# Kernel tuning notes

Hardware: AMD Instinct MI355X
Metric: run time of the kernel (lower is better)

## Reference

```python
import jax, jax.numpy as jnp
import numpy as np

WINDOW_SIZE = 11
SIGMA = 1.5
C1 = 0.01 ** 2
C2 = 0.03 ** 2


def _gaussian_window(window_size: int, channel: int) -> jnp.ndarray:
    # 1D gaussian, normalized
    g = jnp.arange(window_size, dtype=jnp.float32) - window_size // 2
    g = jnp.exp(-(g ** 2) / (2.0 * SIGMA ** 2))
    g = g / g.sum()
    w2d = jnp.outer(g, g)  # [K, K]
    # depthwise conv kernel: [C, 1, K, K] in OIHW with feature_group_count=C
    return jnp.broadcast_to(w2d[None, None], (channel, 1, window_size, window_size))


def _depthwise_conv(x: jnp.ndarray, window: jnp.ndarray, channel: int) -> jnp.ndarray:
    pad = WINDOW_SIZE // 2
    return jax.lax.conv_general_dilated(
        x, window,
        window_strides=(1, 1),
        padding=((pad, pad), (pad, pad)),
        dimension_numbers=('NCHW', 'OIHW', 'NCHW'),
        feature_group_count=channel,
    )


def setup_inputs() -> dict:
    key = jax.random.key(0)
    k1, k2 = jax.random.split(key)
    shape = (16, 3, 512, 512)
    img1 = jax.random.uniform(k1, shape, dtype=jnp.float32)
    img2 = jax.random.uniform(k2, shape, dtype=jnp.float32)
    return {"img1": img1, "img2": img2}


def reference(img1, img2):
    channel = img1.shape[1]
    window = _gaussian_window(WINDOW_SIZE, channel).astype(img1.dtype)

    mu1 = _depthwise_conv(img1, window, channel)
    mu2 = _depthwise_conv(img2, window, channel)

    mu1_sq = mu1 * mu1
    mu2_sq = mu2 * mu2
    mu1_mu2 = mu1 * mu2

    sigma1_sq = _depthwise_conv(img1 * img1, window, channel) - mu1_sq
    sigma2_sq = _depthwise_conv(img2 * img2, window, channel) - mu2_sq
    sigma12 = _depthwise_conv(img1 * img2, window, channel) - mu1_mu2

    ssim_map = ((2.0 * mu1_mu2 + C1) * (2.0 * sigma12 + C2)) / (
        (mu1_sq + mu2_sq + C1) * (sigma1_sq + sigma2_sq + C2))

    return 1.0 - ssim_map.mean()
```

## Files before the change

### kernel.cpp

```cpp
#include <hip/hip_runtime.h>

#define IMG_W 512
#define IMG_H 512
#define PLANE_PX (IMG_W * IMG_H)
#define N_ELEMS (48 * PLANE_PX)
#define NTHREADS 256
#define TILEW 48
#define NCT 11
#define NBANDS 8
#define NBLK (48 * NBANDS * NCT)

#define C1x2 2.0e-4f
#define C2x2 1.8e-3f

typedef _Float16 h2 __attribute__((ext_vector_type(2)));
typedef _Float16 h8 __attribute__((ext_vector_type(8)));
typedef float f32x4 __attribute__((ext_vector_type(4)));
typedef __fp16 fp16v2 __attribute__((ext_vector_type(2)));

__device__ __forceinline__ unsigned int h2bits(h2 v) {
    union { h2 h; unsigned int u; } c; c.h = v; return c.u;
}
__device__ __forceinline__ h2 pkrtz(float x, float y) {
    union { fp16v2 f; h2 h; } c;
    c.f = __builtin_amdgcn_cvt_pkrtz(x, y);
    return c.h;
}

__global__ void __launch_bounds__(NTHREADS, 5) ssim_main(
    const float* __restrict__ img1, const float* __restrict__ img2,
    float* __restrict__ partials)
{
    __shared__ __align__(16) unsigned short P[4 * 64 * 64];

    const int tid = threadIdx.x;
    const int lane = tid & 63;
    const int wv = tid >> 6;
    const int nr = lane & 15;
    const int khi = lane >> 4;

    const int xcd = blockIdx.x & 7;
    const int idx = blockIdx.x >> 3;
    const int pl = xcd * 6 + idx / 88;
    const int t = idx % 88;
    const int band = t / 11;
    const int ct = t - band * 11;
    const int tx0 = ct * TILEW;
    const int ty0 = band * 64;
    const float* pa = img1 + (size_t)pl * PLANE_PX;
    const float* pb = img2 + (size_t)pl * PLANE_PX;

    int sidx = min(lane, 10 - lane);
    unsigned gvb = 0u;
    gvb = (sidx == 0) ? 0x1436u : gvb;
    gvb = (sidx == 1) ? 0x1FC8u : gvb;
    gvb = (sidx == 2) ? 0x289Cu : gvb;
    gvb = (sidx == 3) ? 0x2F00u : gvb;
    gvb = (sidx == 4) ? 0x32D1u : gvb;
    gvb = (sidx == 5) ? 0x3442u : gvb;
    union { h8 h; unsigned u[4]; } af;
#pragma unroll
    for (int w = 0; w < 4; ++w) {
        int t0 = khi * 8 + 2 * w - nr;
        unsigned lo = (unsigned)__shfl((int)gvb, t0 & 63, 64);
        unsigned hi = (unsigned)__shfl((int)gvb, (t0 + 1) & 63, 64);
        af.u[w] = (lo & 0xFFFFu) | (hi << 16);
    }

    const f32x4 z = {0.f, 0.f, 0.f, 0.f};

    const int ry0 = ty0 + wv * 16 - 5;
    const int ryb = ry0 + khi * 8;
    const bool fastY = (ry0 >= 0) && (ry0 + 31 < IMG_H);
    const bool edge = (ct == 0) || (ct == NCT - 1);

#pragma unroll
    for (int tc = 0; tc < 4; ++tc) {
        const int gx = tx0 - 5 + tc * 16 + nr;
        const int cgx = min(max(gx, 0), IMG_W - 1);
        float s[8], d[8];
        if (fastY) {
            const float* qa = pa + (size_t)ryb * IMG_W + cgx;
            const float* qb = pb + (size_t)ryb * IMG_W + cgx;
#pragma unroll
            for (int j = 0; j < 8; ++j) {
                float a = qa[j * IMG_W], b = qb[j * IMG_W];
                s[j] = a + b; d[j] = a - b;
            }
        } else {
#pragma unroll
            for (int j = 0; j < 8; ++j) {
                int ry = ryb + j;
                int ryc = min(max(ry, 0), IMG_H - 1);
                float rm = ((unsigned)ry < (unsigned)IMG_H) ? 1.f : 0.f;
                float a = pa[(size_t)ryc * IMG_W + cgx] * rm;
                float b = pb[(size_t)ryc * IMG_W + cgx] * rm;
                s[j] = a + b; d[j] = a - b;
            }
        }
        union { h8 h; h2 p[4]; } FS, FD, FSS, FDD;
#pragma unroll
        for (int w = 0; w < 4; ++w) {
            FS.p[w] = pkrtz(s[2 * w], s[2 * w + 1]);
            FD.p[w] = pkrtz(d[2 * w], d[2 * w + 1]);
        }
        if (edge) {
            const _Float16 ml = ((unsigned)gx < (unsigned)IMG_W) ? (_Float16)1.f
                                                                 : (_Float16)0.f;
            const h2 mlv = {ml, ml};
#pragma unroll
            for (int w = 0; w < 4; ++w) { FS.p[w] *= mlv; FD.p[w] *= mlv; }
        }
#pragma unroll
        for (int w = 0; w < 4; ++w) {
            FSS.p[w] = FS.p[w] * FS.p[w];
            FDD.p[w] = FD.p[w] * FD.p[w];
        }
        f32x4 oS  = __builtin_amdgcn_mfma_f32_16x16x32_f16(FS.h,  af.h, z, 0, 0, 0);
        f32x4 oD  = __builtin_amdgcn_mfma_f32_16x16x32_f16(FD.h,  af.h, z, 0, 0, 0);
        f32x4 oSS = __builtin_amdgcn_mfma_f32_16x16x32_f16(FSS.h, af.h, z, 0, 0, 0);
        f32x4 oDD = __builtin_amdgcn_mfma_f32_16x16x32_f16(FDD.h, af.h, z, 0, 0, 0);

        const int prow = wv * 16 + nr;
        const int swc = (tc * 16 + khi * 4) ^ ((nr & 7) << 3);
        unsigned short* q = &P[prow * 64 + swc];
        *(uint2*)(q)         = make_uint2(h2bits(pkrtz(oS[0],  oS[1])),
                                          h2bits(pkrtz(oS[2],  oS[3])));
        *(uint2*)(q + 4096)  = make_uint2(h2bits(pkrtz(oD[0],  oD[1])),
                                          h2bits(pkrtz(oD[2],  oD[3])));
        *(uint2*)(q + 8192)  = make_uint2(h2bits(pkrtz(oSS[0], oSS[1])),
                                          h2bits(pkrtz(oSS[2], oSS[3])));
        *(uint2*)(q + 12288) = make_uint2(h2bits(pkrtz(oDD[0], oDD[1])),
                                          h2bits(pkrtz(oDD[2], oDD[3])));
    }
    __syncthreads();

    const int row = wv * 16 + nr;
    float local = 0.f;
#pragma unroll
    for (int mg = 0; mg < 3; ++mg) {
        if (tx0 + mg * 16 < IMG_W) {
            const int gi = ((mg * 2 + khi) ^ (nr & 7)) * 8;
            const unsigned short* base = &P[row * 64 + gi];
            h8 fS  = *(const h8*)(base);
            h8 fD  = *(const h8*)(base + 4096);
            h8 fSS = *(const h8*)(base + 8192);
            h8 fDD = *(const h8*)(base + 12288);
            f32x4 aS  = __builtin_amdgcn_mfma_f32_16x16x32_f16(af.h, fS,  z, 0, 0, 0);
            f32x4 aD  = __builtin_amdgcn_mfma_f32_16x16x32_f16(af.h, fD,  z, 0, 0, 0);
            f32x4 aSS = __builtin_amdgcn_mfma_f32_16x16x32_f16(af.h, fSS, z, 0, 0, 0);
            f32x4 aDD = __builtin_amdgcn_mfma_f32_16x16x32_f16(af.h, fDD, z, 0, 0, 0);

#pragma unroll
            for (int i = 0; i < 4; ++i) {
                float cs = aS[i], cd = aD[i], css = aSS[i], cdd = aDD[i];
                float Pq = cs * cs, Qq = cd * cd;
                float U = Pq - Qq;
                float V = Pq + Qq;
                float num = (U + C1x2) * ((css - cdd) - U + C2x2);
                float den = (V + C1x2) * ((css + cdd) - V + C2x2);
                local += num * __builtin_amdgcn_rcpf(den);
            }
        }
    }

#pragma unroll
    for (int off = 32; off > 0; off >>= 1) local += __shfl_down(local, off, 64);
    __syncthreads();
    float* wp = (float*)P;
    if (lane == 0) wp[wv] = local;
    __syncthreads();
    if (tid == 0)
        partials[blockIdx.x] = wp[0] + wp[1] + wp[2] + wp[3];
}

__global__ void ssim_final(const float* __restrict__ partials,
                           float* __restrict__ out)
{
    __shared__ float wp[4];
    const int tid = threadIdx.x;
    const float4* p4 = (const float4*)partials;
    float s = 0.f;
    for (int i = tid; i < NBLK / 4; i += NTHREADS) {
        float4 v = p4[i];
        s += (v.x + v.y) + (v.z + v.w);
    }
#pragma unroll
    for (int off = 32; off > 0; off >>= 1) s += __shfl_down(s, off, 64);
    if ((tid & 63) == 0) wp[tid >> 6] = s;
    __syncthreads();
    if (tid == 0)
        out[0] = 1.0f - (wp[0] + wp[1] + wp[2] + wp[3]) * (1.0f / (float)N_ELEMS);
}

extern "C" void kernel_launch(void* const* d_in, const int* in_sizes, int n_in,
                              void* d_out, int out_size, void* d_ws, size_t ws_size,
                              hipStream_t stream) {
    const float* img1 = (const float*)d_in[0];
    const float* img2 = (const float*)d_in[1];
    float* out = (float*)d_out;
    float* partials = (float*)d_ws;

    ssim_main<<<NBLK, NTHREADS, 0, stream>>>(img1, img2, partials);
    ssim_final<<<1, NTHREADS, 0, stream>>>(partials, out);
}
```

Baseline: 134.7 us.

## Keep separable blur in registers per wave, removing LDS staging and block sync

Each wave now owns a 16x64 output strip and runs the vertical MFMA on two column groups. It feeds the fp16 results straight back as the B operand of a horizontal MFMA, using a shifted weight fragment, so no shared-memory staging is needed. This removes the LDS round-trip, the __syncthreads barriers and the block-level reduction, and each wave writes its own partial sum. In exchange, halo loads are redundant across the 16-column groups, more global loads are issued per output, and the per-wave loop is not unrolled.

```diff
diff --git a/kernel.cpp b/kernel.cpp
--- a/kernel.cpp
+++ b/kernel.cpp
@@ -5,10 +5,8 @@
 #define PLANE_PX (IMG_W * IMG_H)
 #define N_ELEMS (48 * PLANE_PX)
 #define NTHREADS 256
-#define TILEW 48
-#define NCT 11
-#define NBANDS 8
-#define NBLK (48 * NBANDS * NCT)
+#define NBLK 3072
+#define NWAVES (NBLK * 4)
 
 #define C1x2 2.0e-4f
 #define C2x2 1.8e-3f
@@ -27,26 +25,24 @@
     return c.h;
 }
 
-__global__ void __launch_bounds__(NTHREADS, 5) ssim_main(
+union FrU { h8 h; unsigned u[4]; h2 p[4]; };
+
+__global__ void __launch_bounds__(NTHREADS, 4) ssim_main(
     const float* __restrict__ img1, const float* __restrict__ img2,
     float* __restrict__ partials)
 {
-    __shared__ __align__(16) unsigned short P[4 * 64 * 64];
-
     const int tid = threadIdx.x;
     const int lane = tid & 63;
     const int wv = tid >> 6;
     const int nr = lane & 15;
     const int khi = lane >> 4;
 
-    const int xcd = blockIdx.x & 7;
-    const int idx = blockIdx.x >> 3;
-    const int pl = xcd * 6 + idx / 88;
-    const int t = idx % 88;
-    const int band = t / 11;
-    const int ct = t - band * 11;
-    const int tx0 = ct * TILEW;
-    const int ty0 = band * 64;
+    const int bswz = (blockIdx.x & 7) * (NBLK / 8) + (blockIdx.x >> 3);
+    const int wid = bswz * 4 + wv;
+    const int pl = wid >> 8;
+    const int r = wid & 255;
+    const int oy0 = (r >> 3) * 16;
+    const int sx0 = (r & 7) * 64;
     const float* pa = img1 + (size_t)pl * PLANE_PX;
     const float* pb = img2 + (size_t)pl * PLANE_PX;
 
@@ -58,120 +54,134 @@
     gvb = (sidx == 3) ? 0x2F00u : gvb;
     gvb = (sidx == 4) ? 0x32D1u : gvb;
     gvb = (sidx == 5) ? 0x3442u : gvb;
-    union { h8 h; unsigned u[4]; } af;
+    FrU afv, afh;
 #pragma unroll
     for (int w = 0; w < 4; ++w) {
         int t0 = khi * 8 + 2 * w - nr;
         unsigned lo = (unsigned)__shfl((int)gvb, t0 & 63, 64);
         unsigned hi = (unsigned)__shfl((int)gvb, (t0 + 1) & 63, 64);
-        af.u[w] = (lo & 0xFFFFu) | (hi << 16);
+        afv.u[w] = (lo & 0xFFFFu) | (hi << 16);
+        unsigned lo2 = (unsigned)__shfl((int)gvb, (t0 - 3) & 63, 64);
+        unsigned hi2 = (unsigned)__shfl((int)gvb, (t0 - 2) & 63, 64);
+        afh.u[w] = (lo2 & 0xFFFFu) | (hi2 << 16);
     }
 
+    const int ry0 = oy0 - 5;
+    const int ryb = ry0 + khi * 8;
+    const bool fastY = (ry0 >= 0) && (ry0 + 25 < IMG_H);
+    const int colo = ((nr >> 2) << 3) + (nr & 3);
+
     const f32x4 z = {0.f, 0.f, 0.f, 0.f};
-
-    const int ry0 = ty0 + wv * 16 - 5;
-    const int ryb = ry0 + khi * 8;
-    const bool fastY = (ry0 >= 0) && (ry0 + 31 < IMG_H);
-    const bool edge = (ct == 0) || (ct == NCT - 1);
-
-#pragma unroll
-    for (int tc = 0; tc < 4; ++tc) {
-        const int gx = tx0 - 5 + tc * 16 + nr;
-        const int cgx = min(max(gx, 0), IMG_W - 1);
-        float s[8], d[8];
+    float local = 0.f;
+
+#pragma unroll 1
+    for (int mg = 0; mg < 4; ++mg) {
+        const int ox0 = sx0 + mg * 16;
+        const int wx = ox0 - 8;
+        const int c0 = wx + colo;
+        const int c1 = c0 + 4;
+        const bool edgeC = (wx < 0) || (wx + 32 > IMG_W);
+        const int cc0 = min(max(c0, 0), IMG_W - 1);
+        const int cc1 = min(max(c1, 0), IMG_W - 1);
+
+        float a0[8], b0[8], a1[8], b1[8];
+#pragma unroll
+        for (int j = 0; j < 8; ++j) { a0[j] = 0.f; b0[j] = 0.f; a1[j] = 0.f; b1[j] = 0.f; }
+#define LOADJ_FAST(j) { \
+            a0[j] = qa[(j) * IMG_W + cc0]; b0[j] = qb[(j) * IMG_W + cc0]; \
+            a1[j] = qa[(j) * IMG_W + cc1]; b1[j] = qb[(j) * IMG_W + cc1]; }
+#define LOADJ_EDGE(j) { \
+            int ry = ryb + (j); \
+            int ryc = min(max(ry, 0), IMG_H - 1); \
+            float rm = ((unsigned)ry < (unsigned)IMG_H) ? 1.f : 0.f; \
+            a0[j] = pa[(size_t)ryc * IMG_W + cc0] * rm; \
+            b0[j] = pb[(size_t)ryc * IMG_W + cc0] * rm; \
+            a1[j] = pa[(size_t)ryc * IMG_W + cc1] * rm; \
+            b1[j] = pb[(size_t)ryc * IMG_W + cc1] * rm; }
         if (fastY) {
-            const float* qa = pa + (size_t)ryb * IMG_W + cgx;
-            const float* qb = pb + (size_t)ryb * IMG_W + cgx;
-#pragma unroll
-            for (int j = 0; j < 8; ++j) {
-                float a = qa[j * IMG_W], b = qb[j * IMG_W];
-                s[j] = a + b; d[j] = a - b;
+            const float* qa = pa + (size_t)ryb * IMG_W;
+            const float* qb = pb + (size_t)ryb * IMG_W;
+            LOADJ_FAST(0) LOADJ_FAST(1)
+            if (khi != 3) {
+#pragma unroll
+                for (int j = 2; j < 8; ++j) LOADJ_FAST(j)
             }
         } else {
-#pragma unroll
-            for (int j = 0; j < 8; ++j) {
-                int ry = ryb + j;
-                int ryc = min(max(ry, 0), IMG_H - 1);
-                float rm = ((unsigned)ry < (unsigned)IMG_H) ? 1.f : 0.f;
-                float a = pa[(size_t)ryc * IMG_W + cgx] * rm;
-                float b = pb[(size_t)ryc * IMG_W + cgx] * rm;
-                s[j] = a + b; d[j] = a - b;
+            LOADJ_EDGE(0) LOADJ_EDGE(1)
+            if (khi != 3) {
+#pragma unroll
+                for (int j = 2; j < 8; ++j) LOADJ_EDGE(j)
             }
         }
-        union { h8 h; h2 p[4]; } FS, FD, FSS, FDD;
+#undef LOADJ_FAST
+#undef LOADJ_EDGE
+
+        FrU FS0, FD0, FS1, FD1;
 #pragma unroll
         for (int w = 0; w < 4; ++w) {
-            FS.p[w] = pkrtz(s[2 * w], s[2 * w + 1]);
-            FD.p[w] = pkrtz(d[2 * w], d[2 * w + 1]);
-        }
-        if (edge) {
-            const _Float16 ml = ((unsigned)gx < (unsigned)IMG_W) ? (_Float16)1.f
-                                                                 : (_Float16)0.f;
-            const h2 mlv = {ml, ml};
-#pragma unroll
-            for (int w = 0; w < 4; ++w) { FS.p[w] *= mlv; FD.p[w] *= mlv; }
-        }
+            FS0.p[w] = pkrtz(a0[2 * w] + b0[2 * w], a0[2 * w + 1] + b0[2 * w + 1]);
+            FD0.p[w] = pkrtz(a0[2 * w] - b0[2 * w], a0[2 * w + 1] - b0[2 * w + 1]);
+            FS1.p[w] = pkrtz(a1[2 * w] + b1[2 * w], a1[2 * w + 1] + b1[2 * w + 1]);
+            FD1.p[w] = pkrtz(a1[2 * w] - b1[2 * w], a1[2 * w + 1] - b1[2 * w + 1]);
+        }
+        if (edgeC) {
+            const _Float16 m0 = ((unsigned)c0 < (unsigned)IMG_W) ? (_Float16)1.f : (_Float16)0.f;
+            const _Float16 m1 = ((unsigned)c1 < (unsigned)IMG_W) ? (_Float16)1.f : (_Float16)0.f;
+            const h2 m0v = {m0, m0}, m1v = {m1, m1};
+#pragma unroll
+            for (int w = 0; w < 4; ++w) {
+                FS0.p[w] *= m0v; FD0.p[w] *= m0v;
+                FS1.p[w] *= m1v; FD1.p[w] *= m1v;
+            }
+        }
+        FrU FSS0, FDD0, FSS1, FDD1;
 #pragma unroll
         for (int w = 0; w < 4; ++w) {
-            FSS.p[w] = FS.p[w] * FS.p[w];
-            FDD.p[w] = FD.p[w] * FD.p[w];
-        }
-        f32x4 oS  = __builtin_amdgcn_mfma_f32_16x16x32_f16(FS.h,  af.h, z, 0, 0, 0);
-        f32x4 oD  = __builtin_amdgcn_mfma_f32_16x16x32_f16(FD.h,  af.h, z, 0, 0, 0);
-        f32x4 oSS = __builtin_amdgcn_mfma_f32_16x16x32_f16(FSS.h, af.h, z, 0, 0, 0);
-        f32x4 oDD = __builtin_amdgcn_mfma_f32_16x16x32_f16(FDD.h, af.h, z, 0, 0, 0);
-
-        const int prow = wv * 16 + nr;
-        const int swc = (tc * 16 + khi * 4) ^ ((nr & 7) << 3);
-        unsigned short* q = &P[prow * 64 + swc];
-        *(uint2*)(q)         = make_uint2(h2bits(pkrtz(oS[0],  oS[1])),
-                                          h2bits(pkrtz(oS[2],  oS[3])));
-        *(uint2*)(q + 4096)  = make_uint2(h2bits(pkrtz(oD[0],  oD[1])),
-                                          h2bits(pkrtz(oD[2],  oD[3])));
-        *(uint2*)(q + 8192)  = make_uint2(h2bits(pkrtz(oSS[0], oSS[1])),
-                                          h2bits(pkrtz(oSS[2], oSS[3])));
-        *(uint2*)(q + 12288) = make_uint2(h2bits(pkrtz(oDD[0], oDD[1])),
-                                          h2bits(pkrtz(oDD[2], oDD[3])));
+            FSS0.p[w] = FS0.p[w] * FS0.p[w];
+            FDD0.p[w] = FD0.p[w] * FD0.p[w];
+            FSS1.p[w] = FS1.p[w] * FS1.p[w];
+            FDD1.p[w] = FD1.p[w] * FD1.p[w];
+        }
+
+        f32x4 oS0  = __builtin_amdgcn_mfma_f32_16x16x32_f16(FS0.h,  afv.h, z, 0, 0, 0);
+        f32x4 oD0  = __builtin_amdgcn_mfma_f32_16x16x32_f16(FD0.h,  afv.h, z, 0, 0, 0);
+        f32x4 oSS0 = __builtin_amdgcn_mfma_f32_16x16x32_f16(FSS0.h, afv.h, z, 0, 0, 0);
+        f32x4 oDD0 = __builtin_amdgcn_mfma_f32_16x16x32_f16(FDD0.h, afv.h, z, 0, 0, 0);
+        f32x4 oS1  = __builtin_amdgcn_mfma_f32_16x16x32_f16(FS1.h,  afv.h, z, 0, 0, 0);
+        f32x4 oD1  = __builtin_amdgcn_mfma_f32_16x16x32_f16(FD1.h,  afv.h, z, 0, 0, 0);
+        f32x4 oSS1 = __builtin_amdgcn_mfma_f32_16x16x32_f16(FSS1.h, afv.h, z, 0, 0, 0);
+        f32x4 oDD1 = __builtin_amdgcn_mfma_f32_16x16x32_f16(FDD1.h, afv.h, z, 0, 0, 0);
+
+        FrU bS, bD, bSS, bDD;
+        bS.u[0]  = h2bits(pkrtz(oS0[0],  oS0[1]));  bS.u[1]  = h2bits(pkrtz(oS0[2],  oS0[3]));
+        bS.u[2]  = h2bits(pkrtz(oS1[0],  oS1[1]));  bS.u[3]  = h2bits(pkrtz(oS1[2],  oS1[3]));
+        bD.u[0]  = h2bits(pkrtz(oD0[0],  oD0[1]));  bD.u[1]  = h2bits(pkrtz(oD0[2],  oD0[3]));
+        bD.u[2]  = h2bits(pkrtz(oD1[0],  oD1[1]));  bD.u[3]  = h2bits(pkrtz(oD1[2],  oD1[3]));
+        bSS.u[0] = h2bits(pkrtz(oSS0[0], oSS0[1])); bSS.u[1] = h2bits(pkrtz(oSS0[2], oSS0[3]));
+        bSS.u[2] = h2bits(pkrtz(oSS1[0], oSS1[1])); bSS.u[3] = h2bits(pkrtz(oSS1[2], oSS1[3]));
+        bDD.u[0] = h2bits(pkrtz(oDD0[0], oDD0[1])); bDD.u[1] = h2bits(pkrtz(oDD0[2], oDD0[3]));
+        bDD.u[2] = h2bits(pkrtz(oDD1[0], oDD1[1])); bDD.u[3] = h2bits(pkrtz(oDD1[2], oDD1[3]));
+
+        f32x4 aS  = __builtin_amdgcn_mfma_f32_16x16x32_f16(afh.h, bS.h,  z, 0, 0, 0);
+        f32x4 aD  = __builtin_amdgcn_mfma_f32_16x16x32_f16(afh.h, bD.h,  z, 0, 0, 0);
+        f32x4 aSS = __builtin_amdgcn_mfma_f32_16x16x32_f16(afh.h, bSS.h, z, 0, 0, 0);
+        f32x4 aDD = __builtin_amdgcn_mfma_f32_16x16x32_f16(afh.h, bDD.h, z, 0, 0, 0);
+
+#pragma unroll
+        for (int i = 0; i < 4; ++i) {
+            float cs = aS[i], cd = aD[i], css = aSS[i], cdd = aDD[i];
+            float Pq = cs * cs, Qq = cd * cd;
+            float U = Pq - Qq;
+            float V = Pq + Qq;
+            float num = (U + C1x2) * ((css - cdd) - U + C2x2);
+            float den = (V + C1x2) * ((css + cdd) - V + C2x2);
+            local += num * __builtin_amdgcn_rcpf(den);
+        }
     }
-    __syncthreads();
-
-    const int row = wv * 16 + nr;
-    float local = 0.f;
-#pragma unroll
-    for (int mg = 0; mg < 3; ++mg) {
-        if (tx0 + mg * 16 < IMG_W) {
-            const int gi = ((mg * 2 + khi) ^ (nr & 7)) * 8;
-            const unsigned short* base = &P[row * 64 + gi];
-            h8 fS  = *(const h8*)(base);
-            h8 fD  = *(const h8*)(base + 4096);
-            h8 fSS = *(const h8*)(base + 8192);
-            h8 fDD = *(const h8*)(base + 12288);
-            f32x4 aS  = __builtin_amdgcn_mfma_f32_16x16x32_f16(af.h, fS,  z, 0, 0, 0);
-            f32x4 aD  = __builtin_amdgcn_mfma_f32_16x16x32_f16(af.h, fD,  z, 0, 0, 0);
-            f32x4 aSS = __builtin_amdgcn_mfma_f32_16x16x32_f16(af.h, fSS, z, 0, 0, 0);
-            f32x4 aDD = __builtin_amdgcn_mfma_f32_16x16x32_f16(af.h, fDD, z, 0, 0, 0);
-
-#pragma unroll
-            for (int i = 0; i < 4; ++i) {
-                float cs = aS[i], cd = aD[i], css = aSS[i], cdd = aDD[i];
-                float Pq = cs * cs, Qq = cd * cd;
-                float U = Pq - Qq;
-                float V = Pq + Qq;
-                float num = (U + C1x2) * ((css - cdd) - U + C2x2);
-                float den = (V + C1x2) * ((css + cdd) - V + C2x2);
-                local += num * __builtin_amdgcn_rcpf(den);
-            }
-        }
-    }
 
 #pragma unroll
     for (int off = 32; off > 0; off >>= 1) local += __shfl_down(local, off, 64);
-    __syncthreads();
-    float* wp = (float*)P;
-    if (lane == 0) wp[wv] = local;
-    __syncthreads();
-    if (tid == 0)
-        partials[blockIdx.x] = wp[0] + wp[1] + wp[2] + wp[3];
+    if (lane == 0) partials[wid] = local;
 }
 
 __global__ void ssim_final(const float* __restrict__ partials,
@@ -181,7 +191,7 @@
     const int tid = threadIdx.x;
     const float4* p4 = (const float4*)partials;
     float s = 0.f;
-    for (int i = tid; i < NBLK / 4; i += NTHREADS) {
+    for (int i = tid; i < NWAVES / 4; i += NTHREADS) {
         float4 v = p4[i];
         s += (v.x + v.y) + (v.z + v.w);
     }
```

Result: slower. 155.4 us (+15.3%).

## Retile SSIM blocks to 16-row by 128-column strips with shifted horizontal filter

Applied to the files above, without the earlier changes.

Changes each block from a 64x48 output tile to a 16-row by 128-column strip, giving 6144 blocks. The four waves now split nine 16-column vertical-pass tiles and write them to a padded, unswizzled LDS layout. A second gaussian fragment, shifted by three taps, aligns the horizontal pass to the 8-column halo. The intent is to cut the horizontal halo waste from 48-of-64 columns and to raise occupancy via launch bounds 8 and smaller LDS. In exchange, the vertical halo overhead rises (26 rows loaded per 16 output rows), which means more redundant global reads. The epilogue also uses packed f32x2 math with fma accumulation.

```diff
diff --git a/kernel.cpp b/kernel.cpp
--- a/kernel.cpp
+++ b/kernel.cpp
@@ -4,17 +4,19 @@
 #define IMG_H 512
 #define PLANE_PX (IMG_W * IMG_H)
 #define N_ELEMS (48 * PLANE_PX)
-#define NTHREADS 256
-#define TILEW 48
-#define NCT 11
-#define NBANDS 8
-#define NBLK (48 * NBANDS * NCT)
+#define NT 256
+#define BX 128
+#define NTILE 9
+#define PSTR 152
+#define PPL (16 * PSTR)
+#define NBLK (48 * 32 * 4)
 
 #define C1x2 2.0e-4f
 #define C2x2 1.8e-3f
 
 typedef _Float16 h2 __attribute__((ext_vector_type(2)));
 typedef _Float16 h8 __attribute__((ext_vector_type(8)));
+typedef float f32x2 __attribute__((ext_vector_type(2)));
 typedef float f32x4 __attribute__((ext_vector_type(4)));
 typedef __fp16 fp16v2 __attribute__((ext_vector_type(2)));
 
@@ -27,11 +29,13 @@
     return c.h;
 }
 
-__global__ void __launch_bounds__(NTHREADS, 5) ssim_main(
+union FrU { h8 h; unsigned u[4]; h2 p[4]; };
+
+__global__ void __launch_bounds__(NT, 8) ssim_main(
     const float* __restrict__ img1, const float* __restrict__ img2,
     float* __restrict__ partials)
 {
-    __shared__ __align__(16) unsigned short P[4 * 64 * 64];
+    __shared__ __align__(16) unsigned short P[4 * PPL];
 
     const int tid = threadIdx.x;
     const int lane = tid & 63;
@@ -41,12 +45,12 @@
 
     const int xcd = blockIdx.x & 7;
     const int idx = blockIdx.x >> 3;
-    const int pl = xcd * 6 + idx / 88;
-    const int t = idx % 88;
-    const int band = t / 11;
-    const int ct = t - band * 11;
-    const int tx0 = ct * TILEW;
-    const int ty0 = band * 64;
+    const int pl = xcd * 6 + (idx >> 7);
+    const int rem = idx & 127;
+    const int band = rem >> 2;
+    const int cb = rem & 3;
+    const int bx0 = cb * BX;
+    const int ty0 = band * 16;
     const float* pa = img1 + (size_t)pl * PLANE_PX;
     const float* pb = img2 + (size_t)pl * PLANE_PX;
 
@@ -58,34 +62,35 @@
     gvb = (sidx == 3) ? 0x2F00u : gvb;
     gvb = (sidx == 4) ? 0x32D1u : gvb;
     gvb = (sidx == 5) ? 0x3442u : gvb;
-    union { h8 h; unsigned u[4]; } af;
+    FrU afv, afh;
 #pragma unroll
     for (int w = 0; w < 4; ++w) {
         int t0 = khi * 8 + 2 * w - nr;
         unsigned lo = (unsigned)__shfl((int)gvb, t0 & 63, 64);
         unsigned hi = (unsigned)__shfl((int)gvb, (t0 + 1) & 63, 64);
-        af.u[w] = (lo & 0xFFFFu) | (hi << 16);
+        afv.u[w] = (lo & 0xFFFFu) | (hi << 16);
+        unsigned lo2 = (unsigned)__shfl((int)gvb, (t0 - 3) & 63, 64);
+        unsigned hi2 = (unsigned)__shfl((int)gvb, (t0 - 2) & 63, 64);
+        afh.u[w] = (lo2 & 0xFFFFu) | (hi2 << 16);
     }
 
     const f32x4 z = {0.f, 0.f, 0.f, 0.f};
 
-    const int ry0 = ty0 + wv * 16 - 5;
-    const int ryb = ry0 + khi * 8;
-    const bool fastY = (ry0 >= 0) && (ry0 + 31 < IMG_H);
-    const bool edge = (ct == 0) || (ct == NCT - 1);
-
-#pragma unroll
-    for (int tc = 0; tc < 4; ++tc) {
-        const int gx = tx0 - 5 + tc * 16 + nr;
+    const int ryb = ty0 - 5 + khi * 8;
+    const bool fastY = (ty0 >= 16) && (ty0 <= 480);
+    const bool eb = (cb == 0) || (cb == 3);
+
+    for (int tt = wv; tt < NTILE; tt += 4) {
+        const int gx = bx0 - 8 + tt * 16 + nr;
         const int cgx = min(max(gx, 0), IMG_W - 1);
-        float s[8], d[8];
+        float a[8], b[8];
         if (fastY) {
             const float* qa = pa + (size_t)ryb * IMG_W + cgx;
             const float* qb = pb + (size_t)ryb * IMG_W + cgx;
 #pragma unroll
             for (int j = 0; j < 8; ++j) {
-                float a = qa[j * IMG_W], b = qb[j * IMG_W];
-                s[j] = a + b; d[j] = a - b;
+                a[j] = qa[j * IMG_W];
+                b[j] = qb[j * IMG_W];
             }
         } else {
 #pragma unroll
@@ -93,20 +98,19 @@
                 int ry = ryb + j;
                 int ryc = min(max(ry, 0), IMG_H - 1);
                 float rm = ((unsigned)ry < (unsigned)IMG_H) ? 1.f : 0.f;
-                float a = pa[(size_t)ryc * IMG_W + cgx] * rm;
-                float b = pb[(size_t)ryc * IMG_W + cgx] * rm;
-                s[j] = a + b; d[j] = a - b;
+                a[j] = pa[(size_t)ryc * IMG_W + cgx] * rm;
+                b[j] = pb[(size_t)ryc * IMG_W + cgx] * rm;
             }
         }
-        union { h8 h; h2 p[4]; } FS, FD, FSS, FDD;
+        FrU FS, FD, FSS, FDD;
 #pragma unroll
         for (int w = 0; w < 4; ++w) {
-            FS.p[w] = pkrtz(s[2 * w], s[2 * w + 1]);
-            FD.p[w] = pkrtz(d[2 * w], d[2 * w + 1]);
-        }
-        if (edge) {
-            const _Float16 ml = ((unsigned)gx < (unsigned)IMG_W) ? (_Float16)1.f
-                                                                 : (_Float16)0.f;
+            FS.p[w] = pkrtz(a[2 * w] + b[2 * w], a[2 * w + 1] + b[2 * w + 1]);
+            FD.p[w] = pkrtz(a[2 * w] - b[2 * w], a[2 * w + 1] - b[2 * w + 1]);
+        }
+        if (eb) {
+            const _Float16 ml = ((unsigned)gx < (unsigned)IMG_W)
+                                    ? (_Float16)1.f : (_Float16)0.f;
             const h2 mlv = {ml, ml};
 #pragma unroll
             for (int w = 0; w < 4; ++w) { FS.p[w] *= mlv; FD.p[w] *= mlv; }
@@ -116,53 +120,56 @@
             FSS.p[w] = FS.p[w] * FS.p[w];
             FDD.p[w] = FD.p[w] * FD.p[w];
         }
-        f32x4 oS  = __builtin_amdgcn_mfma_f32_16x16x32_f16(FS.h,  af.h, z, 0, 0, 0);
-        f32x4 oD  = __builtin_amdgcn_mfma_f32_16x16x32_f16(FD.h,  af.h, z, 0, 0, 0);
-        f32x4 oSS = __builtin_amdgcn_mfma_f32_16x16x32_f16(FSS.h, af.h, z, 0, 0, 0);
-        f32x4 oDD = __builtin_amdgcn_mfma_f32_16x16x32_f16(FDD.h, af.h, z, 0, 0, 0);
-
-        const int prow = wv * 16 + nr;
-        const int swc = (tc * 16 + khi * 4) ^ ((nr & 7) << 3);
-        unsigned short* q = &P[prow * 64 + swc];
-        *(uint2*)(q)         = make_uint2(h2bits(pkrtz(oS[0],  oS[1])),
-                                          h2bits(pkrtz(oS[2],  oS[3])));
-        *(uint2*)(q + 4096)  = make_uint2(h2bits(pkrtz(oD[0],  oD[1])),
-                                          h2bits(pkrtz(oD[2],  oD[3])));
-        *(uint2*)(q + 8192)  = make_uint2(h2bits(pkrtz(oSS[0], oSS[1])),
-                                          h2bits(pkrtz(oSS[2], oSS[3])));
-        *(uint2*)(q + 12288) = make_uint2(h2bits(pkrtz(oDD[0], oDD[1])),
-                                          h2bits(pkrtz(oDD[2], oDD[3])));
-    }
-    __syncthreads();
-
-    const int row = wv * 16 + nr;
-    float local = 0.f;
-#pragma unroll
-    for (int mg = 0; mg < 3; ++mg) {
-        if (tx0 + mg * 16 < IMG_W) {
-            const int gi = ((mg * 2 + khi) ^ (nr & 7)) * 8;
-            const unsigned short* base = &P[row * 64 + gi];
-            h8 fS  = *(const h8*)(base);
-            h8 fD  = *(const h8*)(base + 4096);
-            h8 fSS = *(const h8*)(base + 8192);
-            h8 fDD = *(const h8*)(base + 12288);
-            f32x4 aS  = __builtin_amdgcn_mfma_f32_16x16x32_f16(af.h, fS,  z, 0, 0, 0);
-            f32x4 aD  = __builtin_amdgcn_mfma_f32_16x16x32_f16(af.h, fD,  z, 0, 0, 0);
-            f32x4 aSS = __builtin_amdgcn_mfma_f32_16x16x32_f16(af.h, fSS, z, 0, 0, 0);
-            f32x4 aDD = __builtin_amdgcn_mfma_f32_16x16x32_f16(af.h, fDD, z, 0, 0, 0);
-
-#pragma unroll
-            for (int i = 0; i < 4; ++i) {
-                float cs = aS[i], cd = aD[i], css = aSS[i], cdd = aDD[i];
-                float Pq = cs * cs, Qq = cd * cd;
-                float U = Pq - Qq;
-                float V = Pq + Qq;
-                float num = (U + C1x2) * ((css - cdd) - U + C2x2);
-                float den = (V + C1x2) * ((css + cdd) - V + C2x2);
-                local += num * __builtin_amdgcn_rcpf(den);
-            }
-        }
-    }
+        f32x4 oS  = __builtin_amdgcn_mfma_f32_16x16x32_f16(FS.h,  afv.h, z, 0, 0, 0);
+        f32x4 oD  = __builtin_amdgcn_mfma_f32_16x16x32_f16(FD.h,  afv.h, z, 0, 0, 0);
+        f32x4 oSS = __builtin_amdgcn_mfma_f32_16x16x32_f16(FSS.h, afv.h, z, 0, 0, 0);
+        f32x4 oDD = __builtin_amdgcn_mfma_f32_16x16x32_f16(FDD.h, afv.h, z, 0, 0, 0);
+
+        const int wco = nr * PSTR + tt * 16 + khi * 4;
+        *(uint2*)&P[0 * PPL + wco] = make_uint2(h2bits(pkrtz(oS[0],  oS[1])),
+                                                h2bits(pkrtz(oS[2],  oS[3])));
+        *(uint2*)&P[1 * PPL + wco] = make_uint2(h2bits(pkrtz(oD[0],  oD[1])),
+                                                h2bits(pkrtz(oD[2],  oD[3])));
+        *(uint2*)&P[2 * PPL + wco] = make_uint2(h2bits(pkrtz(oSS[0], oSS[1])),
+                                                h2bits(pkrtz(oSS[2], oSS[3])));
+        *(uint2*)&P[3 * PPL + wco] = make_uint2(h2bits(pkrtz(oDD[0], oDD[1])),
+                                                h2bits(pkrtz(oDD[2], oDD[3])));
+    }
+    __syncthreads();
+
+    f32x2 acc2 = {0.f, 0.f};
+    const f32x2 c1v = {C1x2, C1x2};
+    const f32x2 c2v = {C2x2, C2x2};
+#pragma unroll
+    for (int g2 = 0; g2 < 2; ++g2) {
+        const int og = wv * 2 + g2;
+        const int ko = nr * PSTR + og * 16 + khi * 8;
+        h8 fS  = *(const h8*)&P[0 * PPL + ko];
+        h8 fD  = *(const h8*)&P[1 * PPL + ko];
+        h8 fSS = *(const h8*)&P[2 * PPL + ko];
+        h8 fDD = *(const h8*)&P[3 * PPL + ko];
+        f32x4 aS  = __builtin_amdgcn_mfma_f32_16x16x32_f16(afh.h, fS,  z, 0, 0, 0);
+        f32x4 aD  = __builtin_amdgcn_mfma_f32_16x16x32_f16(afh.h, fD,  z, 0, 0, 0);
+        f32x4 aSS = __builtin_amdgcn_mfma_f32_16x16x32_f16(afh.h, fSS, z, 0, 0, 0);
+        f32x4 aDD = __builtin_amdgcn_mfma_f32_16x16x32_f16(afh.h, fDD, z, 0, 0, 0);
+
+#pragma unroll
+        for (int h = 0; h < 2; ++h) {
+            f32x2 cs  = {aS[2 * h],  aS[2 * h + 1]};
+            f32x2 cd  = {aD[2 * h],  aD[2 * h + 1]};
+            f32x2 css = {aSS[2 * h], aSS[2 * h + 1]};
+            f32x2 cdd = {aDD[2 * h], aDD[2 * h + 1]};
+            f32x2 Pq = cs * cs, Qq = cd * cd;
+            f32x2 U = Pq - Qq;
+            f32x2 V = Pq + Qq;
+            f32x2 num = (U + c1v) * ((css - cdd) - U + c2v);
+            f32x2 den = (V + c1v) * ((css + cdd) - V + c2v);
+            f32x2 rr = {__builtin_amdgcn_rcpf(den.x),
+                        __builtin_amdgcn_rcpf(den.y)};
+            acc2 = __builtin_elementwise_fma(num, rr, acc2);
+        }
+    }
+    float local = acc2.x + acc2.y;
 
 #pragma unroll
     for (int off = 32; off > 0; off >>= 1) local += __shfl_down(local, off, 64);
@@ -181,7 +188,7 @@
     const int tid = threadIdx.x;
     const float4* p4 = (const float4*)partials;
     float s = 0.f;
-    for (int i = tid; i < NBLK / 4; i += NTHREADS) {
+    for (int i = tid; i < NBLK / 4; i += NT) {
         float4 v = p4[i];
         s += (v.x + v.y) + (v.z + v.w);
     }
@@ -201,6 +208,6 @@
     float* out = (float*)d_out;
     float* partials = (float*)d_ws;
 
-    ssim_main<<<NBLK, NTHREADS, 0, stream>>>(img1, img2, partials);
-    ssim_final<<<1, NTHREADS, 0, stream>>>(partials, out);
-}
+    ssim_main<<<NBLK, NT, 0, stream>>>(img1, img2, partials);
+    ssim_final<<<1, NT, 0, stream>>>(partials, out);
+}
```

Measured after the change: 147.0 us. +9.1%, slower.
